# Performance work log

Hardware: AMD Instinct MI355X
Metric: run time of the kernel (lower is better)

The kernel has to match this reference:

```python
import jax, jax.numpy as jnp
import numpy as np

HEAD_SIZE = 128
BLOCK_SIZE = 2048


def setup_inputs() -> dict:
    key = jax.random.key(0)
    kx, kk, kq, kv = jax.random.split(key, 4)
    B, T, C = 8, 2048, HEAD_SIZE
    s = 1.0 / np.sqrt(C)
    x = jax.random.normal(kx, (B, T, C), dtype=jnp.float32)
    Wk = jax.random.normal(kk, (C, C), dtype=jnp.float32) * s
    Wq = jax.random.normal(kq, (C, C), dtype=jnp.float32) * s
    Wv = jax.random.normal(kv, (C, C), dtype=jnp.float32) * s
    return {"x": x, "Wk": Wk, "Wq": Wq, "Wv": Wv}


def reference(x, Wk, Wq, Wv):
    B, T, C = x.shape
    # nn.Linear(C, C, bias=False): y = x @ W.T
    k = jnp.einsum('btc,dc->btd', x, Wk)
    q = jnp.einsum('btc,dc->btd', x, Wq)
    v = jnp.einsum('btc,dc->btd', x, Wv)
    scores = jnp.einsum('btd,bsd->bts', q, k) * (C ** -0.5)  # [B,T,T]
    causal = jnp.tril(jnp.ones((T, T), dtype=bool))
    scores = jnp.where(causal, scores, -jnp.inf)
    weights = jax.nn.softmax(scores, axis=-1)
    return jnp.einsum('bts,bsd->btd', weights, v)
```

## Files before the change

### kernel.cpp

```cpp
#include <hip/hip_runtime.h>

#define T_SEQ 2048
#define C_DIM 128

typedef __attribute__((ext_vector_type(8))) short bf16x8;
typedef __attribute__((ext_vector_type(4))) float f32x4;

__device__ __forceinline__ unsigned short f2bf(float f) {
    union { float f; unsigned int u; } v; v.f = f;
    unsigned int r = v.u + 0x7FFFu + ((v.u >> 16) & 1u);
    return (unsigned short)(r >> 16);
}

__global__ __launch_bounds__(256) void proj_kernel(
    const float* __restrict__ x,
    const float* __restrict__ Wq, const float* __restrict__ Wk,
    const float* __restrict__ Wv,
    unsigned short* __restrict__ qo, unsigned short* __restrict__ ko,
    unsigned short* __restrict__ vto)
{
    const int qt = blockIdx.x;
    const int b  = blockIdx.y;
    const int z  = blockIdx.z;
    const int tid  = threadIdx.x;
    const int lane = tid & 63;
    const int w    = tid >> 6;
    const int n16  = lane & 15;
    const int quad = lane >> 4;

    __shared__ __align__(16) unsigned short Wl[128 * 136];
    __shared__ __align__(16) unsigned short Xl[9216];

    const float* W = (z == 0) ? Wq : (z == 1) ? Wk : Wv;

    #pragma unroll
    for (int i = 0; i < 16; ++i) {
        int e = (tid + i * 256) * 4;
        int r = e >> 7, c = e & 127;
        float4 v = *reinterpret_cast<const float4*>(W + r * 128 + c);
        unsigned short* p = &Wl[r * 136 + c];
        p[0] = f2bf(v.x); p[1] = f2bf(v.y); p[2] = f2bf(v.z); p[3] = f2bf(v.w);
    }
    const float* xb = x + ((size_t)b * T_SEQ + (size_t)qt * 64) * C_DIM;
    #pragma unroll
    for (int i = 0; i < 8; ++i) {
        int e = (tid + i * 256) * 4;
        int r = e >> 7, c = e & 127;
        float4 v = *reinterpret_cast<const float4*>(xb + r * 128 + c);
        unsigned short* p = &Xl[r * 136 + c];
        p[0] = f2bf(v.x); p[1] = f2bf(v.y); p[2] = f2bf(v.z); p[3] = f2bf(v.w);
    }
    __syncthreads();

    const int arow = w * 16 + n16;
    bf16x8 afr[4];
    #pragma unroll
    for (int kk = 0; kk < 4; ++kk)
        afr[kk] = *reinterpret_cast<const bf16x8*>(&Xl[arow * 136 + kk * 32 + quad * 8]);

    f32x4 acc[8];
    #pragma unroll
    for (int nt = 0; nt < 8; ++nt) acc[nt] = (f32x4){0.f, 0.f, 0.f, 0.f};

    #pragma unroll
    for (int kk = 0; kk < 4; ++kk) {
        #pragma unroll
        for (int nt = 0; nt < 8; ++nt) {
            bf16x8 bfr = *reinterpret_cast<const bf16x8*>(
                &Wl[(nt * 16 + n16) * 136 + kk * 32 + quad * 8]);
            acc[nt] = __builtin_amdgcn_mfma_f32_16x16x32_bf16(afr[kk], bfr, acc[nt], 0, 0, 0);
        }
    }

    const int trow_base = w * 16 + quad * 4;
    if (z < 2) {
        const float scale = (z == 0) ? 0.08838834764831845f : 1.0f;
        unsigned short* dst = (z == 0 ? qo : ko) +
            ((size_t)b * T_SEQ + (size_t)qt * 64) * C_DIM;
        #pragma unroll
        for (int nt = 0; nt < 8; ++nt)
            #pragma unroll
            for (int r = 0; r < 4; ++r)
                dst[(size_t)(trow_base + r) * C_DIM + nt * 16 + n16] =
                    f2bf(acc[nt][r] * scale);
    } else {
        __syncthreads();
        #pragma unroll
        for (int nt = 0; nt < 8; ++nt)
            #pragma unroll
            for (int r = 0; r < 4; ++r)
                Xl[(nt * 16 + n16) * 72 + trow_base + r] = f2bf(acc[nt][r]);
        __syncthreads();
        unsigned short* dst = vto + (size_t)b * C_DIM * T_SEQ + (size_t)qt * 64;
        #pragma unroll
        for (int i = 0; i < 4; ++i) {
            int e = tid + i * 256;
            int d = e >> 3, cv = (e & 7) * 8;
            *reinterpret_cast<uint4*>(dst + (size_t)d * T_SEQ + cv) =
                *reinterpret_cast<const uint4*>(&Xl[d * 72 + cv]);
        }
    }
}

__global__ __launch_bounds__(256) void attn_kernel(
    const unsigned short* __restrict__ qb,
    const unsigned short* __restrict__ kb,
    const unsigned short* __restrict__ vtb,
    float* __restrict__ out)
{
    const int qt = blockIdx.x;
    const int b  = blockIdx.y;
    const int tid  = threadIdx.x;
    const int lane = tid & 63;
    const int w    = tid >> 6;
    const int n16  = lane & 15;
    const int quad = lane >> 4;

    __shared__ __align__(16) unsigned short Kl[64 * 136];
    __shared__ __align__(16) unsigned short Vl[128 * 72];
    __shared__ __align__(16) unsigned short Pl[4][16 * 72];

    const size_t bT = (size_t)b * T_SEQ;
    const int qbase = qt * 64 + w * 16;

    bf16x8 qfr[4];
    #pragma unroll
    for (int kk = 0; kk < 4; ++kk)
        qfr[kk] = *reinterpret_cast<const bf16x8*>(
            qb + (bT + qbase + n16) * C_DIM + kk * 32 + quad * 8);

    f32x4 o[8];
    #pragma unroll
    for (int ct = 0; ct < 8; ++ct) o[ct] = (f32x4){0.f, 0.f, 0.f, 0.f};
    float m[4], l[4];
    #pragma unroll
    for (int r = 0; r < 4; ++r) { m[r] = -INFINITY; l[r] = 0.f; }

    for (int kt = 0; kt <= qt; ++kt) {
        __syncthreads();
        const unsigned short* ks = kb + (bT + (size_t)kt * 64) * C_DIM;
        #pragma unroll
        for (int i = 0; i < 4; ++i) {
            int e = tid + i * 256;
            int r = e >> 4, c = (e & 15) * 8;
            *reinterpret_cast<uint4*>(&Kl[r * 136 + c]) =
                *reinterpret_cast<const uint4*>(ks + r * 128 + c);
        }
        const unsigned short* vs = vtb + (size_t)b * C_DIM * T_SEQ + (size_t)kt * 64;
        #pragma unroll
        for (int i = 0; i < 4; ++i) {
            int e = tid + i * 256;
            int d = e >> 3, c = (e & 7) * 8;
            *reinterpret_cast<uint4*>(&Vl[d * 72 + c]) =
                *reinterpret_cast<const uint4*>(vs + (size_t)d * T_SEQ + c);
        }
        __syncthreads();

        f32x4 s[4];
        #pragma unroll
        for (int nt = 0; nt < 4; ++nt) s[nt] = (f32x4){0.f, 0.f, 0.f, 0.f};
        #pragma unroll
        for (int kk = 0; kk < 4; ++kk)
            #pragma unroll
            for (int nt = 0; nt < 4; ++nt) {
                bf16x8 bfr = *reinterpret_cast<const bf16x8*>(
                    &Kl[(nt * 16 + n16) * 136 + kk * 32 + quad * 8]);
                s[nt] = __builtin_amdgcn_mfma_f32_16x16x32_bf16(qfr[kk], bfr, s[nt], 0, 0, 0);
            }

        if (kt == qt) {
            #pragma unroll
            for (int nt = 0; nt < 4; ++nt)
                #pragma unroll
                for (int r = 0; r < 4; ++r) {
                    int sabs = kt * 64 + nt * 16 + n16;
                    int qabs = qbase + quad * 4 + r;
                    if (sabs > qabs) s[nt][r] = -1e30f;
                }
        }

        float alpha[4];
        #pragma unroll
        for (int r = 0; r < 4; ++r) {
            float tmax = fmaxf(fmaxf(s[0][r], s[1][r]), fmaxf(s[2][r], s[3][r]));
            #pragma unroll
            for (int off = 1; off < 16; off <<= 1)
                tmax = fmaxf(tmax, __shfl_xor(tmax, off));
            float mn = fmaxf(m[r], tmax);
            alpha[r] = __expf(m[r] - mn);
            float tsum = 0.f;
            #pragma unroll
            for (int nt = 0; nt < 4; ++nt) {
                float p = __expf(s[nt][r] - mn);
                s[nt][r] = p;
                tsum += p;
            }
            #pragma unroll
            for (int off = 1; off < 16; off <<= 1)
                tsum += __shfl_xor(tsum, off);
            l[r] = l[r] * alpha[r] + tsum;
            m[r] = mn;
        }
        #pragma unroll
        for (int ct = 0; ct < 8; ++ct)
            #pragma unroll
            for (int r = 0; r < 4; ++r)
                o[ct][r] *= alpha[r];

        unsigned short* pw = Pl[w];
        #pragma unroll
        for (int nt = 0; nt < 4; ++nt)
            #pragma unroll
            for (int r = 0; r < 4; ++r)
                pw[(quad * 4 + r) * 72 + nt * 16 + n16] = f2bf(s[nt][r]);

        #pragma unroll
        for (int kk2 = 0; kk2 < 2; ++kk2) {
            bf16x8 afr = *reinterpret_cast<const bf16x8*>(
                &pw[n16 * 72 + kk2 * 32 + quad * 8]);
            #pragma unroll
            for (int ct = 0; ct < 8; ++ct) {
                bf16x8 bfr = *reinterpret_cast<const bf16x8*>(
                    &Vl[(ct * 16 + n16) * 72 + kk2 * 32 + quad * 8]);
                o[ct] = __builtin_amdgcn_mfma_f32_16x16x32_bf16(afr, bfr, o[ct], 0, 0, 0);
            }
        }
    }

    float* outp = out + (bT + qbase) * C_DIM;
    #pragma unroll
    for (int r = 0; r < 4; ++r) {
        float inv = 1.0f / l[r];
        #pragma unroll
        for (int ct = 0; ct < 8; ++ct)
            outp[(size_t)(quad * 4 + r) * C_DIM + ct * 16 + n16] = o[ct][r] * inv;
    }
}

extern "C" void kernel_launch(void* const* d_in, const int* in_sizes, int n_in,
                              void* d_out, int out_size, void* d_ws, size_t ws_size,
                              hipStream_t stream) {
    const int B = 8;
    const float* x  = (const float*)d_in[0];
    const float* Wk = (const float*)d_in[1];
    const float* Wq = (const float*)d_in[2];
    const float* Wv = (const float*)d_in[3];

    unsigned short* qw = (unsigned short*)d_ws;
    unsigned short* kw = qw + (size_t)B * T_SEQ * C_DIM;
    unsigned short* vw = kw + (size_t)B * T_SEQ * C_DIM;

    dim3 g1(T_SEQ / 64, B, 3);
    proj_kernel<<<g1, 256, 0, stream>>>(x, Wq, Wk, Wv, qw, kw, vw);

    dim3 g2(T_SEQ / 64, B);
    attn_kernel<<<g2, 256, 0, stream>>>(qw, kw, vw, (float*)d_out);
}
```

Baseline: 139.4 us.

## Split causal attention KV range into chunks with a merge pass and bf16 prep

Splits each query tile's causal key range into chunks of 8 key tiles, processed by separate blocks (split-KV / flash-decoding style). Partial outputs and per-row max/sum go to workspace and are combined by a new merge kernel. This targets load imbalance and low occupancy in the causal attention grid (256 blocks with very uneven work). A prep kernel converts x and the weights to bf16 once, with the QK scale folded into Wq, and the projection now stages results through LDS for coalesced writes. In exchange it adds two kernel launches and extra global traffic for the fp32 partials.

Result: faster. 135.7 us (-2.7%).

```diff
diff --git a/kernel.cpp b/kernel.cpp
--- a/kernel.cpp
+++ b/kernel.cpp
@@ -2,9 +2,15 @@
 
 #define T_SEQ 2048
 #define C_DIM 128
+#define S_QK 0.08838834764831845f
 
 typedef __attribute__((ext_vector_type(8))) short bf16x8;
 typedef __attribute__((ext_vector_type(4))) float f32x4;
+
+#define OPART_OFF 12582912UL
+#define ML_OFF    31457280UL
+#define XBF_OFF   31752192UL
+#define WBF_OFF   35946496UL
 
 __device__ __forceinline__ unsigned short f2bf(float f) {
     union { float f; unsigned int u; } v; v.f = f;
@@ -12,16 +18,49 @@
     return (unsigned short)(r >> 16);
 }
 
+__device__ __forceinline__ int chunk_base(int qt) {
+    int g = qt >> 3;
+    if (g == 1) return (qt - 8) * 2;
+    if (g == 2) return 16 + (qt - 16) * 3;
+    return 40 + (qt - 24) * 4;
+}
+
+__global__ __launch_bounds__(256) void prep_kernel(
+    const float* __restrict__ x,
+    const float* __restrict__ Wk, const float* __restrict__ Wq,
+    const float* __restrict__ Wv,
+    unsigned short* __restrict__ xbf, unsigned short* __restrict__ wbf)
+{
+    int idx = blockIdx.x * 256 + threadIdx.x;
+    const float* src;
+    unsigned short* dst;
+    float scale = 1.0f;
+    if (idx < 524288) {
+        src = x + (size_t)idx * 4;
+        dst = xbf + (size_t)idx * 4;
+    } else {
+        int wi  = idx - 524288;
+        int sel = wi >> 12;
+        int off = (wi & 4095) * 4;
+        src = (sel == 0 ? Wq : sel == 1 ? Wk : Wv) + off;
+        dst = wbf + sel * 16384 + off;
+        if (sel == 0) scale = S_QK;
+    }
+    float4 v = *reinterpret_cast<const float4*>(src);
+    ushort4 o;
+    o.x = f2bf(v.x * scale); o.y = f2bf(v.y * scale);
+    o.z = f2bf(v.z * scale); o.w = f2bf(v.w * scale);
+    *reinterpret_cast<ushort4*>(dst) = o;
+}
+
 __global__ __launch_bounds__(256) void proj_kernel(
-    const float* __restrict__ x,
-    const float* __restrict__ Wq, const float* __restrict__ Wk,
-    const float* __restrict__ Wv,
+    const unsigned short* __restrict__ xbf,
+    const unsigned short* __restrict__ wbf,
     unsigned short* __restrict__ qo, unsigned short* __restrict__ ko,
     unsigned short* __restrict__ vto)
 {
-    const int qt = blockIdx.x;
-    const int b  = blockIdx.y;
-    const int z  = blockIdx.z;
+    const int rt = blockIdx.x;
+    const int z  = blockIdx.y;
     const int tid  = threadIdx.x;
     const int lane = tid & 63;
     const int w    = tid >> 6;
@@ -31,24 +70,21 @@
     __shared__ __align__(16) unsigned short Wl[128 * 136];
     __shared__ __align__(16) unsigned short Xl[9216];
 
-    const float* W = (z == 0) ? Wq : (z == 1) ? Wk : Wv;
-
-    #pragma unroll
-    for (int i = 0; i < 16; ++i) {
-        int e = (tid + i * 256) * 4;
+    const unsigned short* Wsrc = wbf + z * 16384;
+    #pragma unroll
+    for (int i = 0; i < 8; ++i) {
+        int e = (tid + i * 256) * 8;
         int r = e >> 7, c = e & 127;
-        float4 v = *reinterpret_cast<const float4*>(W + r * 128 + c);
-        unsigned short* p = &Wl[r * 136 + c];
-        p[0] = f2bf(v.x); p[1] = f2bf(v.y); p[2] = f2bf(v.z); p[3] = f2bf(v.w);
-    }
-    const float* xb = x + ((size_t)b * T_SEQ + (size_t)qt * 64) * C_DIM;
-    #pragma unroll
-    for (int i = 0; i < 8; ++i) {
-        int e = (tid + i * 256) * 4;
+        *reinterpret_cast<uint4*>(&Wl[r * 136 + c]) =
+            *reinterpret_cast<const uint4*>(Wsrc + e);
+    }
+    const unsigned short* xrow = xbf + (size_t)rt * 64 * C_DIM;
+    #pragma unroll
+    for (int i = 0; i < 4; ++i) {
+        int e = (tid + i * 256) * 8;
         int r = e >> 7, c = e & 127;
-        float4 v = *reinterpret_cast<const float4*>(xb + r * 128 + c);
-        unsigned short* p = &Xl[r * 136 + c];
-        p[0] = f2bf(v.x); p[1] = f2bf(v.y); p[2] = f2bf(v.z); p[3] = f2bf(v.w);
+        *reinterpret_cast<uint4*>(&Xl[r * 136 + c]) =
+            *reinterpret_cast<const uint4*>(xrow + e);
     }
     __syncthreads();
 
@@ -61,30 +97,35 @@
     f32x4 acc[8];
     #pragma unroll
     for (int nt = 0; nt < 8; ++nt) acc[nt] = (f32x4){0.f, 0.f, 0.f, 0.f};
-
-    #pragma unroll
-    for (int kk = 0; kk < 4; ++kk) {
+    #pragma unroll
+    for (int kk = 0; kk < 4; ++kk)
         #pragma unroll
         for (int nt = 0; nt < 8; ++nt) {
             bf16x8 bfr = *reinterpret_cast<const bf16x8*>(
                 &Wl[(nt * 16 + n16) * 136 + kk * 32 + quad * 8]);
             acc[nt] = __builtin_amdgcn_mfma_f32_16x16x32_bf16(afr[kk], bfr, acc[nt], 0, 0, 0);
         }
-    }
 
     const int trow_base = w * 16 + quad * 4;
+    __syncthreads();
     if (z < 2) {
-        const float scale = (z == 0) ? 0.08838834764831845f : 1.0f;
-        unsigned short* dst = (z == 0 ? qo : ko) +
-            ((size_t)b * T_SEQ + (size_t)qt * 64) * C_DIM;
         #pragma unroll
         for (int nt = 0; nt < 8; ++nt)
             #pragma unroll
             for (int r = 0; r < 4; ++r)
-                dst[(size_t)(trow_base + r) * C_DIM + nt * 16 + n16] =
-                    f2bf(acc[nt][r] * scale);
+                Xl[(trow_base + r) * 136 + nt * 16 + n16] = f2bf(acc[nt][r]);
+        __syncthreads();
+        unsigned short* dst = (z == 0 ? qo : ko) + (size_t)rt * 64 * C_DIM;
+        #pragma unroll
+        for (int i = 0; i < 4; ++i) {
+            int e = (tid + i * 256) * 8;
+            int r = e >> 7, c = e & 127;
+            *reinterpret_cast<uint4*>(dst + e) =
+                *reinterpret_cast<const uint4*>(&Xl[r * 136 + c]);
+        }
     } else {
-        __syncthreads();
+        const int b  = rt >> 5;
+        const int qt = rt & 31;
         #pragma unroll
         for (int nt = 0; nt < 8; ++nt)
             #pragma unroll
@@ -106,10 +147,14 @@
     const unsigned short* __restrict__ qb,
     const unsigned short* __restrict__ kb,
     const unsigned short* __restrict__ vtb,
+    float* __restrict__ opart, float2* __restrict__ mlbuf,
     float* __restrict__ out)
 {
-    const int qt = blockIdx.x;
-    const int b  = blockIdx.y;
+    const int qt    = blockIdx.x;
+    const int chunk = blockIdx.y;
+    const int b     = blockIdx.z;
+    if (chunk * 8 > qt) return;
+
     const int tid  = threadIdx.x;
     const int lane = tid & 63;
     const int w    = tid >> 6;
@@ -136,7 +181,10 @@
     #pragma unroll
     for (int r = 0; r < 4; ++r) { m[r] = -INFINITY; l[r] = 0.f; }
 
-    for (int kt = 0; kt <= qt; ++kt) {
+    const int k0 = chunk * 8;
+    const int k1 = min(k0 + 8, qt + 1);
+
+    for (int kt = k0; kt < k1; ++kt) {
         __syncthreads();
         const unsigned short* ks = kb + (bT + (size_t)kt * 64) * C_DIM;
         #pragma unroll
@@ -227,32 +275,89 @@
         }
     }
 
-    float* outp = out + (bT + qbase) * C_DIM;
-    #pragma unroll
-    for (int r = 0; r < 4; ++r) {
-        float inv = 1.0f / l[r];
-        #pragma unroll
-        for (int ct = 0; ct < 8; ++ct)
-            outp[(size_t)(quad * 4 + r) * C_DIM + ct * 16 + n16] = o[ct][r] * inv;
+    if (qt < 8) {
+        float* outp = out + (bT + qbase) * C_DIM;
+        #pragma unroll
+        for (int r = 0; r < 4; ++r) {
+            float inv = 1.0f / l[r];
+            #pragma unroll
+            for (int ct = 0; ct < 8; ++ct)
+                outp[(size_t)(quad * 4 + r) * C_DIM + ct * 16 + n16] = o[ct][r] * inv;
+        }
+    } else {
+        const int slot = b * 72 + chunk_base(qt) + chunk;
+        float* op = opart + (size_t)slot * 8192;
+        #pragma unroll
+        for (int r = 0; r < 4; ++r) {
+            int row = w * 16 + quad * 4 + r;
+            #pragma unroll
+            for (int ct = 0; ct < 8; ++ct)
+                op[row * 128 + ct * 16 + n16] = o[ct][r];
+            if (n16 == 0)
+                mlbuf[(size_t)slot * 64 + row] = make_float2(m[r], l[r]);
+        }
+    }
+}
+
+__global__ __launch_bounds__(256) void merge_kernel(
+    const float* __restrict__ opart, const float2* __restrict__ mlbuf,
+    float* __restrict__ out)
+{
+    const int qt = 8 + blockIdx.x;
+    const int b  = blockIdx.y;
+    const int nch  = (qt >> 3) + 1;
+    const int base = b * 72 + chunk_base(qt);
+    const int row = threadIdx.x >> 2;
+    const int c0  = (threadIdx.x & 3) * 32;
+
+    float mi[4], li[4], wgt[4];
+    float M = -INFINITY;
+    for (int i = 0; i < nch; ++i) {
+        float2 t = mlbuf[(size_t)(base + i) * 64 + row];
+        mi[i] = t.x; li[i] = t.y;
+        M = fmaxf(M, t.x);
+    }
+    float L = 0.f;
+    for (int i = 0; i < nch; ++i) {
+        wgt[i] = __expf(mi[i] - M);
+        L += li[i] * wgt[i];
+    }
+    const float inv = 1.0f / L;
+
+    float* orow = out + ((size_t)(b * T_SEQ + qt * 64 + row)) * C_DIM;
+    #pragma unroll
+    for (int j = 0; j < 8; ++j) {
+        int col = c0 + j * 4;
+        float ax = 0.f, ay = 0.f, az = 0.f, aw = 0.f;
+        for (int i = 0; i < nch; ++i) {
+            float4 p = *reinterpret_cast<const float4*>(
+                opart + (size_t)(base + i) * 8192 + row * 128 + col);
+            ax += wgt[i] * p.x; ay += wgt[i] * p.y;
+            az += wgt[i] * p.z; aw += wgt[i] * p.w;
+        }
+        float4 r4; r4.x = ax * inv; r4.y = ay * inv; r4.z = az * inv; r4.w = aw * inv;
+        *reinterpret_cast<float4*>(orow + col) = r4;
     }
 }
 
 extern "C" void kernel_launch(void* const* d_in, const int* in_sizes, int n_in,
                               void* d_out, int out_size, void* d_ws, size_t ws_size,
                               hipStream_t stream) {
-    const int B = 8;
     const float* x  = (const float*)d_in[0];
     const float* Wk = (const float*)d_in[1];
     const float* Wq = (const float*)d_in[2];
     const float* Wv = (const float*)d_in[3];
 
-    unsigned short* qw = (unsigned short*)d_ws;
-    unsigned short* kw = qw + (size_t)B * T_SEQ * C_DIM;
-    unsigned short* vw = kw + (size_t)B * T_SEQ * C_DIM;
-
-    dim3 g1(T_SEQ / 64, B, 3);
-    proj_kernel<<<g1, 256, 0, stream>>>(x, Wq, Wk, Wv, qw, kw, vw);
-
-    dim3 g2(T_SEQ / 64, B);
-    attn_kernel<<<g2, 256, 0, stream>>>(qw, kw, vw, (float*)d_out);
-}
+    unsigned short* qw  = (unsigned short*)d_ws;
+    unsigned short* kw  = qw + 2097152;
+    unsigned short* vw  = kw + 2097152;
+    float*          opart = (float*)((char*)d_ws + OPART_OFF);
+    float2*         mlb   = (float2*)((char*)d_ws + ML_OFF);
+    unsigned short* xbf   = (unsigned short*)((char*)d_ws + XBF_OFF);
+    unsigned short* wbf   = (unsigned short*)((char*)d_ws + WBF_OFF);
+
+    prep_kernel<<<2096, 256, 0, stream>>>(x, Wk, Wq, Wv, xbf, wbf);
+    proj_kernel<<<dim3(256, 3), 256, 0, stream>>>(xbf, wbf, qw, kw, vw);
+    attn_kernel<<<dim3(32, 4, 8), 256, 0, stream>>>(qw, kw, vw, opart, mlb, (float*)d_out);
+    merge_kernel<<<dim3(24, 8), 256, 0, stream>>>(opart, mlb, (float*)d_out);
+}
```
